# Kernel tuning notes

Hardware: AMD Instinct MI355X
Metric: run time of the kernel (lower is better)

The kernel has to match this reference:

```python
import jax, jax.numpy as jnp
import numpy as np

N = 2708
IN_C = 1433
OUT_C = 64


def setup_inputs() -> dict:
    key = jax.random.key(0)
    k1, k2, k3, k4, k5, k6, k7 = jax.random.split(key, 7)
    X = jax.random.normal(k1, (N, IN_C), dtype=jnp.float32)
    A = jax.random.randint(k2, (N, N), 0, 2, dtype=jnp.int32)  # dense binary adjacency mask
    # Graph Fourier basis: orthonormal-ish random matrix (QR of gaussian)
    U = jnp.linalg.qr(jax.random.normal(k3, (N, N), dtype=jnp.float32))[0]
    s = 1.0 / np.sqrt(IN_C)
    W_K = jax.random.normal(k4, (OUT_C, IN_C), dtype=jnp.float32) * s
    W_Q = jax.random.normal(k5, (OUT_C, IN_C), dtype=jnp.float32) * s
    W_V = jax.random.normal(k6, (OUT_C, IN_C), dtype=jnp.float32) * s
    lmbd = jax.random.uniform(k7, (N, 1), dtype=jnp.float32)
    return {"X": X, "A": A, "U": U, "W_K": W_K, "W_Q": W_Q, "W_V": W_V, "lmbd": lmbd}


def reference(X, A, U, W_K, W_Q, W_V, lmbd):
    # Linear projections (torch nn.Linear: x @ W.T)
    K = X @ W_K.T  # [N, d]
    Q = X @ W_Q.T  # [N, d]
    V = X @ W_V.T  # [N, d]
    d_k = K.shape[-1]
    E = (Q @ K.T) / d_k  # [N, N]
    # spectral filtering: igft(lmbd * gft(E)) = U @ (lmbd * (U^T @ E))
    E = jnp.abs(U @ (lmbd * (U.T @ E)))
    # masked softmax over neighbors; dropout p=0 in eval mode (no-op)
    E_masked = jnp.where(A == 0, -jnp.inf, E)
    alpha = jax.nn.softmax(E_masked, axis=-1)
    H = alpha @ V  # [N, d]
    return H
```

## Files before the change

kernel.cpp:

```cpp
#include <hip/hip_runtime.h>

#define NV 2708
#define INC 1433
#define XCOLS 1472
#define UDIM 2752
#define PSTR 2720
#define BSTR 2752
#define SLAB ((size_t)(2752*64))
#define MWPR 88

typedef __attribute__((ext_vector_type(8))) short bf16x8;
typedef __attribute__((ext_vector_type(4))) float f32x4;
typedef __attribute__((ext_vector_type(4))) unsigned short u16x4;

__device__ __forceinline__ unsigned short f2bf(float f){
  union { float f; unsigned int i; } v; v.f = f;
  return (unsigned short)((v.i + 0x7fffu + ((v.i >> 16) & 1u)) >> 16);
}

__global__ __launch_bounds__(256) void convert_all(
    const float* __restrict__ X, const float* __restrict__ WK,
    const float* __restrict__ WQ, const float* __restrict__ WV,
    const float* __restrict__ U, const int* __restrict__ A,
    unsigned short* __restrict__ Xbf, unsigned short* __restrict__ Wbf,
    unsigned short* __restrict__ Ubf, unsigned int* __restrict__ Abits)
{
  const int bx = blockIdx.x;
  const int tid = threadIdx.x;
  if (bx < 2752){
    const int row = bx;
    unsigned short* dst = Ubf + (size_t)row*UDIM;
    if (row < NV){
      const float* src = U + (size_t)row*NV;
      for (int c4 = tid; c4 < 688; c4 += 256){
        float4 v = make_float4(0.f,0.f,0.f,0.f);
        if (c4 < 677) v = *(const float4*)(src + c4*4);
        u16x4 h = { f2bf(v.x), f2bf(v.y), f2bf(v.z), f2bf(v.w) };
        *(u16x4*)(dst + c4*4) = h;
      }
    } else {
      u16x4 zz = {0,0,0,0};
      for (int c4 = tid; c4 < 688; c4 += 256) *(u16x4*)(dst + c4*4) = zz;
    }
  } else if (bx < 5504){
    const int row = bx - 2752;
    unsigned short* dst = Xbf + (size_t)row*XCOLS;
    if (row < NV){
      const float* src = X + (size_t)row*INC;
      for (int c = tid; c < XCOLS; c += 256)
        dst[c] = (c < INC) ? f2bf(src[c]) : (unsigned short)0;
    } else {
      for (int c = tid; c < XCOLS; c += 256) dst[c] = 0;
    }
  } else if (bx < 5696){
    const int row = bx - 5504;
    const float* s = (row < 64) ? WK : (row < 128) ? WQ : WV;
    const float* src = s + (size_t)(row & 63)*INC;
    unsigned short* dst = Wbf + (size_t)row*XCOLS;
    for (int c = tid; c < XCOLS; c += 256)
      dst[c] = (c < INC) ? f2bf(src[c]) : (unsigned short)0;
  } else {
    const int i = bx - 5696;
    const int lane = tid & 63, wave = tid >> 6;
    const int* arow = A + (size_t)i*NV;
    unsigned int* drow = Abits + (size_t)i*MWPR;
    if (tid < 2) drow[86 + tid] = 0u;
    for (int g = wave; g < 43; g += 4){
      int j = g*64 + lane;
      int a = (j < NV) ? arow[j] : 0;
      unsigned long long m = __ballot(a != 0);
      if (lane == 0){
        drow[2*g]     = (unsigned int)m;
        drow[2*g + 1] = (unsigned int)(m >> 32);
      }
    }
  }
}

__global__ __launch_bounds__(256) void proj(
    const unsigned short* __restrict__ Xbf, const unsigned short* __restrict__ Wbf,
    float* __restrict__ part)
{
  __shared__ __align__(16) unsigned short At[64*72];
  __shared__ __align__(16) unsigned short Bt[64*72];
  const int tid = threadIdx.x;
  const int lane = tid & 63, wave = tid >> 6, quad = lane >> 4, lr = lane & 15;
  const int m0 = blockIdx.x * 64;
  const int s  = blockIdx.y, z = blockIdx.z;
  const int kbeg = s * 384, kend = min(kbeg + 384, XCOLS);
  const int wm = (wave & 1) * 32, wn = (wave >> 1) * 32;
  const unsigned short* Wz = Wbf + (size_t)z*64*XCOLS;
  const int srow = wave*8 + (lane >> 3), seg = lane & 7;
  f32x4 acc[2][2] = {};

  for (int k0 = kbeg; k0 < kend; k0 += 64){
    #pragma unroll
    for (int e = 0; e < 2; e++){
      int row = e*32 + srow;
      bf16x8 xa = *(const bf16x8*)(Xbf + (size_t)(m0+row)*XCOLS + k0 + seg*8);
      bf16x8 wb = *(const bf16x8*)(Wz  + (size_t)row*XCOLS      + k0 + seg*8);
      *(bf16x8*)&At[row*72 + seg*8] = xa;
      *(bf16x8*)&Bt[row*72 + seg*8] = wb;
    }
    __syncthreads();
    #pragma unroll
    for (int ks = 0; ks < 2; ks++){
      bf16x8 af[2], bv[2];
      #pragma unroll
      for (int t = 0; t < 2; t++){
        af[t] = *(const bf16x8*)&At[(wm + t*16 + lr)*72 + ks*32 + quad*8];
        bv[t] = *(const bf16x8*)&Bt[(wn + t*16 + lr)*72 + ks*32 + quad*8];
      }
      #pragma unroll
      for (int tm = 0; tm < 2; tm++)
        #pragma unroll
        for (int tn = 0; tn < 2; tn++)
          acc[tm][tn] = __builtin_amdgcn_mfma_f32_16x16x32_bf16(af[tm], bv[tn], acc[tm][tn], 0, 0, 0);
    }
    __syncthreads();
  }
  float* dst = part + (size_t)(z*4 + s) * SLAB;
  #pragma unroll
  for (int tm = 0; tm < 2; tm++)
    #pragma unroll
    for (int tn = 0; tn < 2; tn++)
      #pragma unroll
      for (int e = 0; e < 4; e++)
        dst[(size_t)(m0 + wm + tm*16 + quad*4 + e)*64 + wn + tn*16 + lr] = acc[tm][tn][e];
}

__global__ __launch_bounds__(256) void reduce_proj(
    const float* __restrict__ part, unsigned short* __restrict__ K16f,
    unsigned short* __restrict__ QT16, unsigned short* __restrict__ VTf)
{
  int idx = blockIdx.x*256 + threadIdx.x;
  int z = blockIdx.y;
  int m = idx >> 6, c = idx & 63;
  const float* base = part + (size_t)z*4*SLAB + idx;
  float v = 0.f;
  #pragma unroll
  for (int s = 0; s < 4; s++) v += base[s*SLAB];
  unsigned short h = (m < NV) ? f2bf(v) : (unsigned short)0;
  if (z == 0){
    if (m < 2720) K16f[((m>>4)*2 + (c>>5))*512 + (m&15)*32 + (c&31)] = h;
  } else if (z == 1){
    QT16[(size_t)c*BSTR + m] = h;
  } else {
    if (m < 2720) VTf[(m>>5)*2048 + c*32 + (m&31)] = h;
  }
}

__global__ __launch_bounds__(256) void gemmG(
    const unsigned short* __restrict__ Ubf, const unsigned short* __restrict__ QT,
    float* __restrict__ part)
{
  __shared__ __align__(16) unsigned short At[64*72];
  __shared__ __align__(16) unsigned short Bt[64*72];
  const int tid = threadIdx.x;
  const int lane = tid & 63, wave = tid >> 6, quad = lane >> 4, lr = lane & 15;
  const int m0 = blockIdx.x * 64;
  const int s  = blockIdx.y;
  const int kbeg = s * 192, kend = min(kbeg + 192, UDIM);
  const int wm = (wave & 1) * 32, wn = (wave >> 1) * 32;
  const int bc = tid >> 2, bseg = tid & 3;
  const int ml = (lane & 15)*4, koff = wave*16 + (lane >> 4);
  f32x4 acc[2][2] = {};

  for (int k0 = kbeg; k0 < kend; k0 += 64){
    #pragma unroll
    for (int e = 0; e < 4; e++){
      int kl = koff + e*4;
      u16x4 v = *(const u16x4*)(Ubf + (size_t)(k0+kl)*UDIM + m0 + ml);
      At[(ml+0)*72 + kl] = v[0];
      At[(ml+1)*72 + kl] = v[1];
      At[(ml+2)*72 + kl] = v[2];
      At[(ml+3)*72 + kl] = v[3];
    }
    {
      const unsigned short* q = QT + (size_t)bc*BSTR + k0 + bseg*16;
      *(bf16x8*)&Bt[bc*72 + bseg*16]     = *(const bf16x8*)(q);
      *(bf16x8*)&Bt[bc*72 + bseg*16 + 8] = *(const bf16x8*)(q + 8);
    }
    __syncthreads();
    #pragma unroll
    for (int ks = 0; ks < 2; ks++){
      bf16x8 af[2], bv[2];
      #pragma unroll
      for (int t = 0; t < 2; t++){
        af[t] = *(const bf16x8*)&At[(wm + t*16 + lr)*72 + ks*32 + quad*8];
        bv[t] = *(const bf16x8*)&Bt[(wn + t*16 + lr)*72 + ks*32 + quad*8];
      }
      #pragma unroll
      for (int tm = 0; tm < 2; tm++)
        #pragma unroll
        for (int tn = 0; tn < 2; tn++)
          acc[tm][tn] = __builtin_amdgcn_mfma_f32_16x16x32_bf16(af[tm], bv[tn], acc[tm][tn], 0, 0, 0);
    }
    __syncthreads();
  }
  float* dst = part + (size_t)s * SLAB;
  #pragma unroll
  for (int tm = 0; tm < 2; tm++)
    #pragma unroll
    for (int tn = 0; tn < 2; tn++)
      #pragma unroll
      for (int e = 0; e < 4; e++)
        dst[(size_t)(m0 + wm + tm*16 + quad*4 + e)*64 + wn + tn*16 + lr] = acc[tm][tn][e];
}

__global__ __launch_bounds__(256) void reduce_g(
    const float* __restrict__ part, const float* __restrict__ lm,
    unsigned short* __restrict__ G2T)
{
  int idx = blockIdx.x*256 + threadIdx.x;
  int m = idx >> 6, c = idx & 63;
  const float* base = part + idx;
  float v = 0.f;
  #pragma unroll
  for (int s = 0; s < 15; s++) v += base[s*SLAB];
  unsigned short h = 0;
  if (m < NV) h = f2bf(v * lm[m] * (1.0f/64.0f));
  G2T[(size_t)c*BSTR + m] = h;
}

__global__ __launch_bounds__(256) void gemmF(
    const unsigned short* __restrict__ Ubf, const unsigned short* __restrict__ G2T,
    float* __restrict__ part)
{
  __shared__ __align__(16) unsigned short At[64*72];
  __shared__ __align__(16) unsigned short Bt[64*72];
  const int tid = threadIdx.x;
  const int lane = tid & 63, wave = tid >> 6, quad = lane >> 4, lr = lane & 15;
  const int m0 = blockIdx.x * 64;
  const int s  = blockIdx.y;
  const int kbeg = s * 192, kend = min(kbeg + 192, UDIM);
  const int wm = (wave & 1) * 32, wn = (wave >> 1) * 32;
  const int bc = tid >> 2, bseg = tid & 3;
  const int srow = wave*8 + (lane >> 3), seg = lane & 7;
  f32x4 acc[2][2] = {};

  for (int k0 = kbeg; k0 < kend; k0 += 64){
    #pragma unroll
    for (int e = 0; e < 2; e++){
      int row = e*32 + srow;
      bf16x8 ua = *(const bf16x8*)(Ubf + (size_t)(m0+row)*UDIM + k0 + seg*8);
      *(bf16x8*)&At[row*72 + seg*8] = ua;
    }
    {
      const unsigned short* g = G2T + (size_t)bc*BSTR + k0 + bseg*16;
      *(bf16x8*)&Bt[bc*72 + bseg*16]     = *(const bf16x8*)(g);
      *(bf16x8*)&Bt[bc*72 + bseg*16 + 8] = *(const bf16x8*)(g + 8);
    }
    __syncthreads();
    #pragma unroll
    for (int ks = 0; ks < 2; ks++){
      bf16x8 af[2], bv[2];
      #pragma unroll
      for (int t = 0; t < 2; t++){
        af[t] = *(const bf16x8*)&At[(wm + t*16 + lr)*72 + ks*32 + quad*8];
        bv[t] = *(const bf16x8*)&Bt[(wn + t*16 + lr)*72 + ks*32 + quad*8];
      }
      #pragma unroll
      for (int tm = 0; tm < 2; tm++)
        #pragma unroll
        for (int tn = 0; tn < 2; tn++)
          acc[tm][tn] = __builtin_amdgcn_mfma_f32_16x16x32_bf16(af[tm], bv[tn], acc[tm][tn], 0, 0, 0);
    }
    __syncthreads();
  }
  float* dst = part + (size_t)s * SLAB;
  #pragma unroll
  for (int tm = 0; tm < 2; tm++)
    #pragma unroll
    for (int tn = 0; tn < 2; tn++)
      #pragma unroll
      for (int e = 0; e < 4; e++)
        dst[(size_t)(m0 + wm + tm*16 + quad*4 + e)*64 + wn + tn*16 + lr] = acc[tm][tn][e];
}

__global__ __launch_bounds__(256) void reduce_f(
    const float* __restrict__ part, unsigned short* __restrict__ F16)
{
  int idx = blockIdx.x*256 + threadIdx.x;
  int m = idx >> 6;
  const float* base = part + idx;
  float v = 0.f;
  #pragma unroll
  for (int s = 0; s < 15; s++) v += base[s*SLAB];
  F16[idx] = (m < NV) ? f2bf(v) : (unsigned short)0;
}

__global__ __launch_bounds__(256) void fused_attn(
    const unsigned short* __restrict__ F16, const unsigned short* __restrict__ K16f,
    const unsigned int* __restrict__ Abits, const unsigned short* __restrict__ VTf,
    float* __restrict__ Hout)
{
  __shared__ __align__(16) unsigned short pbuf[8*PSTR];
  __shared__ unsigned int mrow[8*MWPR];
  __shared__ float swave[4][8];
  __shared__ float rinv[8];
  const int tid  = threadIdx.x;
  const int lane = tid & 63, wave = tid >> 6;
  const int quad = lane >> 4, lr = lane & 15;
  const int i0 = blockIdx.x * 8;

  for (int idx = tid; idx < 8*MWPR; idx += 256){
    int r = idx / MWPR;
    unsigned int v = 0;
    if (i0 + r < NV) v = Abits[(size_t)(i0 + r)*MWPR + (idx - r*MWPR)];
    mrow[idx] = v;
  }
  __syncthreads();

  const unsigned short* frow = F16 + (size_t)(i0 + (lr & 7))*64;
  bf16x8 af0 = *(const bf16x8*)(frow + quad*8);
  bf16x8 af1 = *(const bf16x8*)(frow + 32 + quad*8);
  float psum[4] = {0.f, 0.f, 0.f, 0.f};
  for (int t = wave; t < 170; t += 4){
    const unsigned short* kb = K16f + t*1024 + lr*32 + quad*8;
    bf16x8 b0 = *(const bf16x8*)(kb);
    bf16x8 b1 = *(const bf16x8*)(kb + 512);
    f32x4 sv = {};
    sv = __builtin_amdgcn_mfma_f32_16x16x32_bf16(af0, b0, sv, 0, 0, 0);
    sv = __builtin_amdgcn_mfma_f32_16x16x32_bf16(af1, b1, sv, 0, 0, 0);
    if (quad < 2){
      int col = t*16 + lr;
      int wsh = col >> 5, bit = col & 31;
      #pragma unroll
      for (int e = 0; e < 4; e++){
        int r = quad*4 + e;
        float p = 0.f;
        if ((mrow[r*MWPR + wsh] >> bit) & 1u) p = __expf(fabsf(sv[e]));
        psum[e] += p;
        pbuf[r*PSTR + col] = f2bf(p);
      }
    }
  }
  #pragma unroll
  for (int e = 0; e < 4; e++){
    float v = psum[e];
    #pragma unroll
    for (int o = 1; o <= 8; o <<= 1) v += __shfl_xor(v, o, 64);
    if (lr == 0 && quad < 2) swave[wave][quad*4 + e] = v;
  }
  __syncthreads();
  if (tid < 8){
    float sum = swave[0][tid] + swave[1][tid] + swave[2][tid] + swave[3][tid];
    rinv[tid] = (sum > 0.f) ? (1.f/sum) : 0.f;
  }
  __syncthreads();

  const int c0 = wave * 16;
  const int mr = lr & 7;
  f32x4 acc = {};
  for (int kt = 0; kt < 85; kt++){
    bf16x8 af = *(const bf16x8*)&pbuf[mr*PSTR + kt*32 + quad*8];
    bf16x8 bv = *(const bf16x8*)&VTf[kt*2048 + (c0 + lr)*32 + quad*8];
    acc = __builtin_amdgcn_mfma_f32_16x16x32_bf16(af, bv, acc, 0, 0, 0);
  }
  if (quad < 2){
    #pragma unroll
    for (int e = 0; e < 4; e++){
      int r = quad*4 + e;
      int i = i0 + r;
      if (i < NV) Hout[(size_t)i*64 + c0 + lr] = acc[e] * rinv[r];
    }
  }
}

extern "C" void kernel_launch(void* const* d_in, const int* in_sizes, int n_in,
                              void* d_out, int out_size, void* d_ws, size_t ws_size,
                              hipStream_t stream){
  (void)in_sizes; (void)n_in; (void)out_size; (void)ws_size;
  const float* X  = (const float*)d_in[0];
  const int*   A  = (const int*)d_in[1];
  const float* U  = (const float*)d_in[2];
  const float* WK = (const float*)d_in[3];
  const float* WQ = (const float*)d_in[4];
  const float* WV = (const float*)d_in[5];
  const float* lm = (const float*)d_in[6];

  char* ws = (char*)d_ws;
  size_t off = 0;
  auto alloc = [&](size_t bytes){ size_t o = off; off = (off + bytes + 255) & ~(size_t)255; return o; };
  float*          part = (float*)(ws + alloc(15*SLAB*4));
  unsigned short* Ubf  = (unsigned short*)(ws + alloc((size_t)UDIM*UDIM*2));
  unsigned short* Xbf  = (unsigned short*)(ws + alloc((size_t)UDIM*XCOLS*2));
  unsigned short* Wbf  = (unsigned short*)(ws + alloc((size_t)192*XCOLS*2));
  unsigned short* K16f = (unsigned short*)(ws + alloc((size_t)170*1024*2));
  unsigned short* QT16 = (unsigned short*)(ws + alloc((size_t)64*BSTR*2));
  unsigned short* G2T  = (unsigned short*)(ws + alloc((size_t)64*BSTR*2));
  unsigned short* VTf  = (unsigned short*)(ws + alloc((size_t)85*2048*2));
  unsigned short* F16  = (unsigned short*)(ws + alloc((size_t)2720*64*2));
  unsigned int*   Abits= (unsigned int*)(ws + alloc((size_t)NV*MWPR*4));

  convert_all<<<dim3(8404), 256, 0, stream>>>(X, WK, WQ, WV, U, A, Xbf, Wbf, Ubf, Abits);
  proj<<<dim3(43, 4, 3), 256, 0, stream>>>(Xbf, Wbf, part);
  reduce_proj<<<dim3(688, 3), 256, 0, stream>>>(part, K16f, QT16, VTf);
  gemmG<<<dim3(43, 15), 256, 0, stream>>>(Ubf, QT16, part);
  reduce_g<<<dim3(688), 256, 0, stream>>>(part, lm, G2T);
  gemmF<<<dim3(43, 15), 256, 0, stream>>>(Ubf, G2T, part);
  reduce_f<<<dim3(680), 256, 0, stream>>>(part, F16);
  fused_attn<<<dim3((NV + 7)/8), 256, 0, stream>>>(F16, K16f, Abits, VTf, (float*)d_out);
}
```

Before: 197.8 us.

## Raise split-K counts, fuse F reduction into attention, prefetch K/V tiles

The split-K factor goes up, to 8 for the projection GEMM and 22 for the two U GEMMs, so more workgroups fill the GPU. The separate reduce_f kernel is removed: fused_attn now sums the 22 partial slabs for its 8 rows directly into shared memory, which saves one launch and one intermediate buffer. The K and V tile loads in the attention loops are software-prefetched one iteration ahead to hide global-memory latency. The cost is more partial-sum traffic (24 slabs) and more adds in the reductions.

```diff
diff --git a/kernel.cpp b/kernel.cpp
--- a/kernel.cpp
+++ b/kernel.cpp
@@ -8,6 +8,8 @@
 #define BSTR 2752
 #define SLAB ((size_t)(2752*64))
 #define MWPR 88
+#define NSP 8
+#define NSU 22
 
 typedef __attribute__((ext_vector_type(8))) short bf16x8;
 typedef __attribute__((ext_vector_type(4))) float f32x4;
@@ -87,7 +89,7 @@
   const int lane = tid & 63, wave = tid >> 6, quad = lane >> 4, lr = lane & 15;
   const int m0 = blockIdx.x * 64;
   const int s  = blockIdx.y, z = blockIdx.z;
-  const int kbeg = s * 384, kend = min(kbeg + 384, XCOLS);
+  const int kbeg = s * 192, kend = min(kbeg + 192, XCOLS);
   const int wm = (wave & 1) * 32, wn = (wave >> 1) * 32;
   const unsigned short* Wz = Wbf + (size_t)z*64*XCOLS;
   const int srow = wave*8 + (lane >> 3), seg = lane & 7;
@@ -119,7 +121,7 @@
     }
     __syncthreads();
   }
-  float* dst = part + (size_t)(z*4 + s) * SLAB;
+  float* dst = part + (size_t)(z*NSP + s) * SLAB;
   #pragma unroll
   for (int tm = 0; tm < 2; tm++)
     #pragma unroll
@@ -136,10 +138,10 @@
   int idx = blockIdx.x*256 + threadIdx.x;
   int z = blockIdx.y;
   int m = idx >> 6, c = idx & 63;
-  const float* base = part + (size_t)z*4*SLAB + idx;
+  const float* base = part + (size_t)z*NSP*SLAB + idx;
   float v = 0.f;
   #pragma unroll
-  for (int s = 0; s < 4; s++) v += base[s*SLAB];
+  for (int s = 0; s < NSP; s++) v += base[s*SLAB];
   unsigned short h = (m < NV) ? f2bf(v) : (unsigned short)0;
   if (z == 0){
     if (m < 2720) K16f[((m>>4)*2 + (c>>5))*512 + (m&15)*32 + (c&31)] = h;
@@ -160,7 +162,7 @@
   const int lane = tid & 63, wave = tid >> 6, quad = lane >> 4, lr = lane & 15;
   const int m0 = blockIdx.x * 64;
   const int s  = blockIdx.y;
-  const int kbeg = s * 192, kend = min(kbeg + 192, UDIM);
+  const int kbeg = s * 128, kend = min(kbeg + 128, UDIM);
   const int wm = (wave & 1) * 32, wn = (wave >> 1) * 32;
   const int bc = tid >> 2, bseg = tid & 3;
   const int ml = (lane & 15)*4, koff = wave*16 + (lane >> 4);
@@ -217,7 +219,7 @@
   const float* base = part + idx;
   float v = 0.f;
   #pragma unroll
-  for (int s = 0; s < 15; s++) v += base[s*SLAB];
+  for (int s = 0; s < NSU; s++) v += base[s*SLAB];
   unsigned short h = 0;
   if (m < NV) h = f2bf(v * lm[m] * (1.0f/64.0f));
   G2T[(size_t)c*BSTR + m] = h;
@@ -233,7 +235,7 @@
   const int lane = tid & 63, wave = tid >> 6, quad = lane >> 4, lr = lane & 15;
   const int m0 = blockIdx.x * 64;
   const int s  = blockIdx.y;
-  const int kbeg = s * 192, kend = min(kbeg + 192, UDIM);
+  const int kbeg = s * 128, kend = min(kbeg + 128, UDIM);
   const int wm = (wave & 1) * 32, wn = (wave >> 1) * 32;
   const int bc = tid >> 2, bseg = tid & 3;
   const int srow = wave*8 + (lane >> 3), seg = lane & 7;
@@ -278,24 +280,13 @@
         dst[(size_t)(m0 + wm + tm*16 + quad*4 + e)*64 + wn + tn*16 + lr] = acc[tm][tn][e];
 }
 
-__global__ __launch_bounds__(256) void reduce_f(
-    const float* __restrict__ part, unsigned short* __restrict__ F16)
-{
-  int idx = blockIdx.x*256 + threadIdx.x;
-  int m = idx >> 6;
-  const float* base = part + idx;
-  float v = 0.f;
-  #pragma unroll
-  for (int s = 0; s < 15; s++) v += base[s*SLAB];
-  F16[idx] = (m < NV) ? f2bf(v) : (unsigned short)0;
-}
-
 __global__ __launch_bounds__(256) void fused_attn(
-    const unsigned short* __restrict__ F16, const unsigned short* __restrict__ K16f,
+    const float* __restrict__ partF, const unsigned short* __restrict__ K16f,
     const unsigned int* __restrict__ Abits, const unsigned short* __restrict__ VTf,
     float* __restrict__ Hout)
 {
   __shared__ __align__(16) unsigned short pbuf[8*PSTR];
+  __shared__ __align__(16) unsigned short fbuf[8*64];
   __shared__ unsigned int mrow[8*MWPR];
   __shared__ float swave[4][8];
   __shared__ float rinv[8];
@@ -304,6 +295,15 @@
   const int quad = lane >> 4, lr = lane & 15;
   const int i0 = blockIdx.x * 8;
 
+  #pragma unroll
+  for (int h = 0; h < 2; h++){
+    int idx = h*256 + tid;
+    const float* base = partF + (size_t)(i0 + (idx >> 6))*64 + (idx & 63);
+    float v = 0.f;
+    #pragma unroll
+    for (int s = 0; s < NSU; s++) v += base[s*SLAB];
+    fbuf[idx] = f2bf(v);
+  }
   for (int idx = tid; idx < 8*MWPR; idx += 256){
     int r = idx / MWPR;
     unsigned int v = 0;
@@ -312,28 +312,38 @@
   }
   __syncthreads();
 
-  const unsigned short* frow = F16 + (size_t)(i0 + (lr & 7))*64;
-  bf16x8 af0 = *(const bf16x8*)(frow + quad*8);
-  bf16x8 af1 = *(const bf16x8*)(frow + 32 + quad*8);
+  const bf16x8 af0 = *(const bf16x8*)&fbuf[(lr & 7)*64 + quad*8];
+  const bf16x8 af1 = *(const bf16x8*)&fbuf[(lr & 7)*64 + 32 + quad*8];
   float psum[4] = {0.f, 0.f, 0.f, 0.f};
-  for (int t = wave; t < 170; t += 4){
+  {
+    int t = wave;
     const unsigned short* kb = K16f + t*1024 + lr*32 + quad*8;
     bf16x8 b0 = *(const bf16x8*)(kb);
     bf16x8 b1 = *(const bf16x8*)(kb + 512);
-    f32x4 sv = {};
-    sv = __builtin_amdgcn_mfma_f32_16x16x32_bf16(af0, b0, sv, 0, 0, 0);
-    sv = __builtin_amdgcn_mfma_f32_16x16x32_bf16(af1, b1, sv, 0, 0, 0);
-    if (quad < 2){
-      int col = t*16 + lr;
-      int wsh = col >> 5, bit = col & 31;
-      #pragma unroll
-      for (int e = 0; e < 4; e++){
-        int r = quad*4 + e;
-        float p = 0.f;
-        if ((mrow[r*MWPR + wsh] >> bit) & 1u) p = __expf(fabsf(sv[e]));
-        psum[e] += p;
-        pbuf[r*PSTR + col] = f2bf(p);
-      }
+    while (t < 170){
+      int tn = t + 4;
+      bf16x8 n0 = b0, n1 = b1;
+      if (tn < 170){
+        const unsigned short* nb = K16f + tn*1024 + lr*32 + quad*8;
+        n0 = *(const bf16x8*)(nb);
+        n1 = *(const bf16x8*)(nb + 512);
+      }
+      f32x4 sv = {};
+      sv = __builtin_amdgcn_mfma_f32_16x16x32_bf16(af0, b0, sv, 0, 0, 0);
+      sv = __builtin_amdgcn_mfma_f32_16x16x32_bf16(af1, b1, sv, 0, 0, 0);
+      if (quad < 2){
+        int col = t*16 + lr;
+        int wsh = col >> 5, bit = col & 31;
+        #pragma unroll
+        for (int e = 0; e < 4; e++){
+          int r = quad*4 + e;
+          float p = 0.f;
+          if ((mrow[r*MWPR + wsh] >> bit) & 1u) p = __expf(fabsf(sv[e]));
+          psum[e] += p;
+          pbuf[r*PSTR + col] = f2bf(p);
+        }
+      }
+      b0 = n0; b1 = n1; t = tn;
     }
   }
   #pragma unroll
@@ -353,10 +363,15 @@
   const int c0 = wave * 16;
   const int mr = lr & 7;
   f32x4 acc = {};
-  for (int kt = 0; kt < 85; kt++){
-    bf16x8 af = *(const bf16x8*)&pbuf[mr*PSTR + kt*32 + quad*8];
-    bf16x8 bv = *(const bf16x8*)&VTf[kt*2048 + (c0 + lr)*32 + quad*8];
-    acc = __builtin_amdgcn_mfma_f32_16x16x32_bf16(af, bv, acc, 0, 0, 0);
+  {
+    bf16x8 bv = *(const bf16x8*)&VTf[(c0 + lr)*32 + quad*8];
+    for (int kt = 0; kt < 85; kt++){
+      bf16x8 bn = bv;
+      if (kt + 1 < 85) bn = *(const bf16x8*)&VTf[(kt+1)*2048 + (c0 + lr)*32 + quad*8];
+      bf16x8 af = *(const bf16x8*)&pbuf[mr*PSTR + kt*32 + quad*8];
+      acc = __builtin_amdgcn_mfma_f32_16x16x32_bf16(af, bv, acc, 0, 0, 0);
+      bv = bn;
+    }
   }
   if (quad < 2){
     #pragma unroll
@@ -383,7 +398,7 @@
   char* ws = (char*)d_ws;
   size_t off = 0;
   auto alloc = [&](size_t bytes){ size_t o = off; off = (off + bytes + 255) & ~(size_t)255; return o; };
-  float*          part = (float*)(ws + alloc(15*SLAB*4));
+  float*          part = (float*)(ws + alloc(24*SLAB*4));
   unsigned short* Ubf  = (unsigned short*)(ws + alloc((size_t)UDIM*UDIM*2));
   unsigned short* Xbf  = (unsigned short*)(ws + alloc((size_t)UDIM*XCOLS*2));
   unsigned short* Wbf  = (unsigned short*)(ws + alloc((size_t)192*XCOLS*2));
@@ -391,15 +406,13 @@
   unsigned short* QT16 = (unsigned short*)(ws + alloc((size_t)64*BSTR*2));
   unsigned short* G2T  = (unsigned short*)(ws + alloc((size_t)64*BSTR*2));
   unsigned short* VTf  = (unsigned short*)(ws + alloc((size_t)85*2048*2));
-  unsigned short* F16  = (unsigned short*)(ws + alloc((size_t)2720*64*2));
   unsigned int*   Abits= (unsigned int*)(ws + alloc((size_t)NV*MWPR*4));
 
   convert_all<<<dim3(8404), 256, 0, stream>>>(X, WK, WQ, WV, U, A, Xbf, Wbf, Ubf, Abits);
-  proj<<<dim3(43, 4, 3), 256, 0, stream>>>(Xbf, Wbf, part);
+  proj<<<dim3(43, NSP, 3), 256, 0, stream>>>(Xbf, Wbf, part);
   reduce_proj<<<dim3(688, 3), 256, 0, stream>>>(part, K16f, QT16, VTf);
-  gemmG<<<dim3(43, 15), 256, 0, stream>>>(Ubf, QT16, part);
+  gemmG<<<dim3(43, NSU), 256, 0, stream>>>(Ubf, QT16, part);
   reduce_g<<<dim3(688), 256, 0, stream>>>(part, lm, G2T);
-  gemmF<<<dim3(43, 15), 256, 0, stream>>>(Ubf, G2T, part);
-  reduce_f<<<dim3(680), 256, 0, stream>>>(part, F16);
-  fused_attn<<<dim3((NV + 7)/8), 256, 0, stream>>>(F16, K16f, Abits, VTf, (float*)d_out);
-}
+  gemmF<<<dim3(43, NSU), 256, 0, stream>>>(Ubf, G2T, part);
+  fused_attn<<<dim3((NV + 7)/8), 256, 0, stream>>>(part, K16f, Abits, VTf, (float*)d_out);
+}
```

Result: no change. 196.7 us (-0.6%).
